# Performance work log

Measured on AMD Instinct MI355X. Metric: run time of the kernel, lower is better.

The kernel has to match this reference:

```python
import jax, jax.numpy as jnp
import numpy as np

NUM_E = 1024
E_DIM = 64
BETA = 0.5


def setup_inputs() -> dict:
    key = jax.random.key(0)
    k1, k2 = jax.random.split(key)
    z_e = jax.random.normal(k1, (32, E_DIM, 64, 64), dtype=jnp.float32)  # [B, C, H, W]
    codebook = jax.random.uniform(k2, (NUM_E, E_DIM), dtype=jnp.float32,
                                  minval=-1.0 / NUM_E, maxval=1.0 / NUM_E)
    return {"z_e": z_e, "codebook": codebook}


def reference(z_e, codebook):
    B, C, H, W = z_e.shape
    sg = jax.lax.stop_gradient
    z = jnp.transpose(z_e, (0, 2, 3, 1))            # [B, H, W, C]
    zf = z.reshape(-1, C)                           # [N, C]
    # squared L2 distances via ||z||^2 + ||e||^2 - 2 z.e  -> [N, num_e]
    d = (jnp.sum(zf * zf, axis=1, keepdims=True)
         + jnp.sum(codebook * codebook, axis=1)
         - 2.0 * jnp.matmul(zf, codebook.T))
    idx = jnp.argmin(d, axis=1)                     # [N]
    z_q = codebook[idx].reshape(z.shape)            # gather instead of one-hot matmul
    loss = jnp.mean((sg(z_q) - z) ** 2) + BETA * jnp.mean((z_q - sg(z)) ** 2)
    z_q_st = z + sg(z_q - z)                        # straight-through
    # code usage histogram == mean of one-hot encodings
    counts = jnp.zeros((NUM_E,), dtype=z.dtype).at[idx].add(1.0)
    e_mean = counts / idx.shape[0]
    perplexity = jnp.exp(-jnp.sum(e_mean * jnp.log(e_mean + 1e-10)))
    z_q_out = jnp.transpose(z_q_st, (0, 3, 1, 2))   # back to [B, C, H, W]
    return (z_q_out, loss, sg(perplexity), idx.reshape(B, H, W))
```

## Files before the change

### kernel.cpp

```cpp
#include <hip/hip_runtime.h>
#include <math.h>

#define NUM_E   1024
#define ZQ_ELEM 8388608
#define AGRID   1024
#define QCAP    2048

typedef short bf16x8 __attribute__((ext_vector_type(8)));
typedef float f32x16 __attribute__((ext_vector_type(16)));

__device__ inline unsigned short rne_bf16(float v) {
    unsigned u = __float_as_uint(v);
    return (unsigned short)((u + 0x7FFFu + ((u >> 16) & 1u)) >> 16);
}

__global__ __launch_bounds__(256) void vq_prep(const float* __restrict__ cb,
                                               float* __restrict__ ee,
                                               unsigned short* __restrict__ ehi)
{
    int j = blockIdx.x * 256 + threadIdx.x;
    const float* r = cb + (size_t)j * 64;
    float v[64];
#pragma unroll
    for (int k = 0; k < 64; ++k) v[k] = r[k];
    float a = 0.f;
#pragma unroll
    for (int k = 0; k < 64; ++k) a = fmaf(v[k], v[k], a);
    ee[j] = a;

    int nt = j >> 5, jc = j & 31;
#pragma unroll
    for (int kt = 0; kt < 4; ++kt)
#pragma unroll
        for (int h = 0; h < 2; ++h) {
            bf16x8 vh;
#pragma unroll
            for (int i = 0; i < 8; ++i)
                vh[i] = (short)rne_bf16(v[kt * 16 + h * 8 + i]);
            *(bf16x8*)(ehi + ((size_t)(nt * 4 + kt) * 64 + h * 32 + jc) * 8) = vh;
        }
}

__device__ inline void refine_one(const float* zb, const float* zzs,
                                  const float* ee, const float* cb,
                                  unsigned long long* best, int pl, int j)
{
    const float4* cr = (const float4*)(cb + ((size_t)j << 6));
    float a = 0.f;
#pragma unroll
    for (int q = 0; q < 16; ++q) {
        float4 c4 = cr[q];
        a = fmaf(zb[(size_t)(4 * q + 0) * 4096 + pl], c4.x, a);
        a = fmaf(zb[(size_t)(4 * q + 1) * 4096 + pl], c4.y, a);
        a = fmaf(zb[(size_t)(4 * q + 2) * 4096 + pl], c4.z, a);
        a = fmaf(zb[(size_t)(4 * q + 3) * 4096 + pl], c4.w, a);
    }
    float t1 = zzs[pl] + ee[j];
    float d  = fmaf(-2.f, a, t1);
    unsigned long long key =
        ((unsigned long long)__float_as_uint(d) << 32) | (unsigned long long)j;
    atomicMin(best + pl, key);
}

#define LOADB(H, EV, ntv) do {                                      \
    int _b = (ntv) * 4 * 64 + lane;                                 \
    _Pragma("unroll")                                               \
    for (int _k = 0; _k < 4; ++_k) H[_k] = eh8[_b + _k * 64];       \
    EV = ee[(ntv) * 32 + (lane & 31)];                              \
} while (0)

__global__ __launch_bounds__(256, 4) void vq_argmin(
    const float* __restrict__ z, const float* __restrict__ cb,
    const unsigned short* __restrict__ ehi, const float* __restrict__ ee,
    float* __restrict__ idx_f, int* __restrict__ counts,
    float* __restrict__ zq, double* __restrict__ partials)
{
    __shared__ float zzs[128];
    __shared__ float wp[128];
    __shared__ unsigned long long best[128];
    __shared__ unsigned int queue[QCAP];
    __shared__ unsigned int qcnt;
    __shared__ unsigned int oflow;
    __shared__ int ibuf[128];
    __shared__ double wsum[4];

    const int tid  = threadIdx.x;
    const int g    = blockIdx.x;
    const int lane = tid & 63, wv = tid >> 6;
    const size_t zoff = ((size_t)(g >> 5) << 18) + (size_t)((g & 31) << 7);
    const float* zb = z + zoff;
    const bf16x8* eh8 = (const bf16x8*)ehi;

    if (tid < 128) best[tid] = 0xFFFFFFFFFFFFFFFFull;
    if (tid == 0) { qcnt = 0; oflow = 0; }

    if (tid < 128) {
        float vv[64];
#pragma unroll
        for (int k = 0; k < 64; ++k) vv[k] = zb[(size_t)k * 4096 + tid];
        float a = 0.f;
#pragma unroll
        for (int k = 0; k < 64; ++k) a = fmaf(vv[k], vv[k], a);
        zzs[tid] = a;
    }

    bf16x8 ah[4];
    {
        int h = lane >> 5;
        int pl = wv * 32 + (lane & 31);
        float s1 = 0.f, sd = 0.f;
#pragma unroll
        for (int kt = 0; kt < 4; ++kt)
#pragma unroll
            for (int i = 0; i < 8; ++i) {
                int k = kt * 16 + h * 8 + i;
                float x = zb[(size_t)k * 4096 + pl];
                unsigned short hb = rne_bf16(x);
                float hf = __uint_as_float((unsigned)hb << 16);
                ah[kt][i] = (short)hb;
                s1 += fabsf(x);
                sd += fabsf(x - hf);
            }
        s1 += __shfl_xor(s1, 32);
        sd += __shfl_xor(sd, 32);
        if (lane < 32) wp[pl] = 4.f * (s1 * 1.907e-6f + sd * 9.785e-4f) + 1.4e-4f;
    }
    __syncthreads();

    float m[16];
#pragma unroll
    for (int r = 0; r < 16; ++r) m[r] = 3.4e38f;

    bf16x8 hA[4], hB[4];
    float  eA, eB;

    LOADB(hA, eA, 0);
#pragma unroll 1
    for (int nt = 0; nt < 32; nt += 2) {
        LOADB(hB, eB, nt + 1);
        {
            f32x16 acc;
#pragma unroll
            for (int r = 0; r < 16; ++r) acc[r] = 0.f;
#pragma unroll
            for (int kt = 0; kt < 4; ++kt)
                acc = __builtin_amdgcn_mfma_f32_32x32x16_bf16(ah[kt], hA[kt], acc, 0, 0, 0);
#pragma unroll
            for (int r = 0; r < 16; ++r) m[r] = fminf(m[r], fmaf(-2.f, acc[r], eA));
        }
        if (nt + 2 < 32) LOADB(hA, eA, nt + 2);
        {
            f32x16 acc;
#pragma unroll
            for (int r = 0; r < 16; ++r) acc[r] = 0.f;
#pragma unroll
            for (int kt = 0; kt < 4; ++kt)
                acc = __builtin_amdgcn_mfma_f32_32x32x16_bf16(ah[kt], hB[kt], acc, 0, 0, 0);
#pragma unroll
            for (int r = 0; r < 16; ++r) m[r] = fminf(m[r], fmaf(-2.f, acc[r], eB));
        }
    }
#pragma unroll
    for (int r = 0; r < 16; ++r) {
        for (int d2 = 1; d2 <= 16; d2 <<= 1)
            m[r] = fminf(m[r], __shfl_xor(m[r], d2));
        m[r] += wp[wv * 32 + 4 * (lane >> 5) + (r & 3) + 8 * (r >> 2)];
    }

    LOADB(hA, eA, 0);
#pragma unroll 1
    for (int nt = 0; nt < 32; nt += 2) {
        LOADB(hB, eB, nt + 1);
        {
            f32x16 acc;
#pragma unroll
            for (int r = 0; r < 16; ++r) acc[r] = 0.f;
#pragma unroll
            for (int kt = 0; kt < 4; ++kt)
                acc = __builtin_amdgcn_mfma_f32_32x32x16_bf16(ah[kt], hA[kt], acc, 0, 0, 0);
            unsigned jj = (unsigned)(nt * 32 + (lane & 31));
#pragma unroll
            for (int r = 0; r < 16; ++r) {
                bool hit = fmaf(-2.f, acc[r], eA) <= m[r];
                if (__any(hit)) {
                    if (hit) {
                        int pl = wv * 32 + 4 * (lane >> 5) + (r & 3) + 8 * (r >> 2);
                        unsigned slot = atomicAdd(&qcnt, 1u);
                        if (slot < QCAP) queue[slot] = ((unsigned)pl << 16) | jj;
                        else oflow = 1;
                    }
                }
            }
        }
        if (nt + 2 < 32) LOADB(hA, eA, nt + 2);
        {
            f32x16 acc;
#pragma unroll
            for (int r = 0; r < 16; ++r) acc[r] = 0.f;
#pragma unroll
            for (int kt = 0; kt < 4; ++kt)
                acc = __builtin_amdgcn_mfma_f32_32x32x16_bf16(ah[kt], hB[kt], acc, 0, 0, 0);
            unsigned jj = (unsigned)((nt + 1) * 32 + (lane & 31));
#pragma unroll
            for (int r = 0; r < 16; ++r) {
                bool hit = fmaf(-2.f, acc[r], eB) <= m[r];
                if (__any(hit)) {
                    if (hit) {
                        int pl = wv * 32 + 4 * (lane >> 5) + (r & 3) + 8 * (r >> 2);
                        unsigned slot = atomicAdd(&qcnt, 1u);
                        if (slot < QCAP) queue[slot] = ((unsigned)pl << 16) | jj;
                        else oflow = 1;
                    }
                }
            }
        }
    }
    __syncthreads();

    if (oflow) {
        if (tid < 128)
            for (int j = 0; j < NUM_E; ++j) refine_one(zb, zzs, ee, cb, best, tid, j);
    } else {
        int nq = (int)qcnt;
        for (int e = tid; e < nq; e += 256) {
            unsigned u = queue[e];
            refine_one(zb, zzs, ee, cb, best, (int)(u >> 16), (int)(u & 0xFFFFu));
        }
    }
    __syncthreads();
    if (tid < 128) {
        int bi = (int)(best[tid] & 0xFFFFFFFFull);
        ibuf[tid] = bi;
        idx_f[(size_t)g * 128 + tid] = (float)bi;
        atomicAdd(&counts[bi], 1);
    }
    __syncthreads();

    {
        int w4 = tid & 31, c8 = (tid >> 5) * 8;
        const float4* zb4 = (const float4*)zb;
        float4* zq4 = (float4*)(zq + zoff);
        size_t b0 = (size_t)ibuf[w4 * 4 + 0] << 6;
        size_t b1 = (size_t)ibuf[w4 * 4 + 1] << 6;
        size_t b2 = (size_t)ibuf[w4 * 4 + 2] << 6;
        size_t b3 = (size_t)ibuf[w4 * 4 + 3] << 6;
        double ls = 0.0;
#pragma unroll
        for (int i = 0; i < 8; ++i) {
            int c = c8 + i;
            float4 zv = zb4[(size_t)c * 1024 + w4];
            float q0 = cb[b0 + c], q1 = cb[b1 + c], q2 = cb[b2 + c], q3 = cb[b3 + c];
            float t0 = q0 - zv.x, t1 = q1 - zv.y, t2 = q2 - zv.z, t3 = q3 - zv.w;
            zq4[(size_t)c * 1024 + w4] =
                make_float4(zv.x + t0, zv.y + t1, zv.z + t2, zv.w + t3);
            ls += (double)t0 * t0 + (double)t1 * t1 + (double)t2 * t2 + (double)t3 * t3;
        }
#pragma unroll
        for (int off = 32; off > 0; off >>= 1) ls += __shfl_down(ls, off);
        if ((tid & 63) == 0) wsum[tid >> 6] = ls;
    }
    __syncthreads();
    if (tid == 0) partials[g] = wsum[0] + wsum[1] + wsum[2] + wsum[3];
}

__global__ __launch_bounds__(256) void vq_final(
    const int* __restrict__ counts, const double* __restrict__ partials,
    float* __restrict__ scalars)
{
    __shared__ double sh[256];
    __shared__ double sl[256];
    int t = threadIdx.x;
    double s = 0.0;
    for (int j = t; j < NUM_E; j += 256) {
        float em   = (float)counts[j] * (1.0f / 131072.0f);
        float term = em * logf(em + 1e-10f);
        s += (double)term;
    }
    double l = 0.0;
#pragma unroll
    for (int j = 0; j < AGRID / 256; ++j) l += partials[j * 256 + t];
    sh[t] = s;
    sl[t] = l;
    __syncthreads();
    for (int off = 128; off > 0; off >>= 1) {
        if (t < off) { sh[t] += sh[t + off]; sl[t] += sl[t + off]; }
        __syncthreads();
    }
    if (t == 0) {
        float mm = (float)(sl[0] / 8388608.0);
        scalars[0] = mm + 0.5f * mm;
        scalars[1] = expf(-(float)sh[0]);
    }
}

extern "C" void kernel_launch(void* const* d_in, const int* in_sizes, int n_in,
                              void* d_out, int out_size, void* d_ws, size_t ws_size,
                              hipStream_t stream)
{
    const float* z  = (const float*)d_in[0];
    const float* cb = (const float*)d_in[1];
    float* out     = (float*)d_out;
    float* zq      = out;
    float* scalars = out + ZQ_ELEM;
    float* idx_f   = out + ZQ_ELEM + 2;

    int*            counts   = (int*)d_ws;
    double*         partials = (double*)((char*)d_ws + 4096);
    float*          ee       = (float*)((char*)d_ws + 12288);
    unsigned short* ehi      = (unsigned short*)((char*)d_ws + 16384);

    hipMemsetAsync(d_ws, 0, 4096, stream);
    vq_prep  <<<4,     256, 0, stream>>>(cb, ee, ehi);
    vq_argmin<<<AGRID, 256, 0, stream>>>(z, cb, ehi, ee, idx_f, counts, zq, partials);
    vq_final <<<1,     256, 0, stream>>>(counts, partials, scalars);
}
```

Baseline: 111.9 us.

## Stage bf16 codebook in LDS, widen blocks to 512 points with per-point candidate lists

```diff
diff --git a/kernel.cpp b/kernel.cpp
--- a/kernel.cpp
+++ b/kernel.cpp
@@ -3,8 +3,9 @@
 
 #define NUM_E   1024
 #define ZQ_ELEM 8388608
-#define AGRID   1024
-#define QCAP    2048
+#define AGRID   256
+#define MAXC    7
+#define OQCAP   512
 
 typedef short bf16x8 __attribute__((ext_vector_type(8)));
 typedef float f32x16 __attribute__((ext_vector_type(16)));
@@ -41,9 +42,26 @@
         }
 }
 
-__device__ inline void refine_one(const float* zb, const float* zzs,
-                                  const float* ee, const float* cb,
-                                  unsigned long long* best, int pl, int j)
+__device__ inline unsigned long long key_regs(const float* vv, float zz, float eej,
+                                              const float* cb, int j)
+{
+    const float4* cr = (const float4*)(cb + ((size_t)j << 6));
+    float a = 0.f;
+#pragma unroll
+    for (int q = 0; q < 16; ++q) {
+        float4 c4 = cr[q];
+        a = fmaf(vv[4 * q + 0], c4.x, a);
+        a = fmaf(vv[4 * q + 1], c4.y, a);
+        a = fmaf(vv[4 * q + 2], c4.z, a);
+        a = fmaf(vv[4 * q + 3], c4.w, a);
+    }
+    float t1 = zz + eej;
+    float d  = fmaf(-2.f, a, t1);
+    return ((unsigned long long)__float_as_uint(d) << 32) | (unsigned long long)j;
+}
+
+__device__ inline unsigned long long key_glob(const float* zb, float zz, float eej,
+                                              const float* cb, int pl, int j)
 {
     const float4* cr = (const float4*)(cb + ((size_t)j << 6));
     float a = 0.f;
@@ -55,212 +73,220 @@
         a = fmaf(zb[(size_t)(4 * q + 2) * 4096 + pl], c4.z, a);
         a = fmaf(zb[(size_t)(4 * q + 3) * 4096 + pl], c4.w, a);
     }
-    float t1 = zzs[pl] + ee[j];
+    float t1 = zz + eej;
     float d  = fmaf(-2.f, a, t1);
-    unsigned long long key =
-        ((unsigned long long)__float_as_uint(d) << 32) | (unsigned long long)j;
-    atomicMin(best + pl, key);
-}
-
-#define LOADB(H, EV, ntv) do {                                      \
-    int _b = (ntv) * 4 * 64 + lane;                                 \
-    _Pragma("unroll")                                               \
-    for (int _k = 0; _k < 4; ++_k) H[_k] = eh8[_b + _k * 64];       \
-    EV = ee[(ntv) * 32 + (lane & 31)];                              \
-} while (0)
-
-__global__ __launch_bounds__(256, 4) void vq_argmin(
+    return ((unsigned long long)__float_as_uint(d) << 32) | (unsigned long long)j;
+}
+
+__global__ __launch_bounds__(512, 2) void vq_argmin(
     const float* __restrict__ z, const float* __restrict__ cb,
     const unsigned short* __restrict__ ehi, const float* __restrict__ ee,
     float* __restrict__ idx_f, int* __restrict__ counts,
     float* __restrict__ zq, double* __restrict__ partials)
 {
-    __shared__ float zzs[128];
-    __shared__ float wp[128];
-    __shared__ unsigned long long best[128];
-    __shared__ unsigned int queue[QCAP];
-    __shared__ unsigned int qcnt;
-    __shared__ unsigned int oflow;
-    __shared__ int ibuf[128];
-    __shared__ double wsum[4];
+    __shared__ bf16x8 bB[8192];
+    __shared__ float  eeL[1024];
+    __shared__ float  zzsL[512];
+    __shared__ float  wp[512];
+    __shared__ unsigned long long best[512];
+    __shared__ unsigned short cand[512 * MAXC];
+    __shared__ unsigned int ccnt[512];
+    __shared__ unsigned int oq[OQCAP];
+    __shared__ unsigned int oqcnt, gflow;
+    __shared__ double wsum[8];
 
     const int tid  = threadIdx.x;
     const int g    = blockIdx.x;
     const int lane = tid & 63, wv = tid >> 6;
-    const size_t zoff = ((size_t)(g >> 5) << 18) + (size_t)((g & 31) << 7);
+    const size_t zoff = ((size_t)(g >> 3) << 18) + (size_t)((g & 7) << 9);
     const float* zb = z + zoff;
-    const bf16x8* eh8 = (const bf16x8*)ehi;
-
-    if (tid < 128) best[tid] = 0xFFFFFFFFFFFFFFFFull;
-    if (tid == 0) { qcnt = 0; oflow = 0; }
-
-    if (tid < 128) {
-        float vv[64];
-#pragma unroll
-        for (int k = 0; k < 64; ++k) vv[k] = zb[(size_t)k * 4096 + tid];
+
+    best[tid] = 0xFFFFFFFFFFFFFFFFull;
+    ccnt[tid] = 0;
+    if (tid == 0) { oqcnt = 0; gflow = 0; }
+    eeL[tid]       = ee[tid];
+    eeL[tid + 512] = ee[tid + 512];
+
+    {
+        const uint4* src = (const uint4*)ehi;
+        uint4* dst = (uint4*)bB;
+#pragma unroll
+        for (int pass = 0; pass < 4; ++pass) {
+            uint4 a = src[pass * 2048 + tid];
+            uint4 b = src[pass * 2048 + 512 + tid];
+            uint4 c = src[pass * 2048 + 1024 + tid];
+            uint4 d = src[pass * 2048 + 1536 + tid];
+            dst[pass * 2048 + tid] = a;
+            dst[pass * 2048 + 512 + tid] = b;
+            dst[pass * 2048 + 1024 + tid] = c;
+            dst[pass * 2048 + 1536 + tid] = d;
+        }
+    }
+
+    float vv[64];
+#pragma unroll
+    for (int k = 0; k < 64; ++k) vv[k] = zb[(size_t)k * 4096 + tid];
+    float zz;
+    {
         float a = 0.f;
 #pragma unroll
         for (int k = 0; k < 64; ++k) a = fmaf(vv[k], vv[k], a);
-        zzs[tid] = a;
-    }
-
-    bf16x8 ah[4];
+        zz = a; zzsL[tid] = a;
+    }
+
+    bf16x8 ah0[4], ah1[4];
     {
         int h = lane >> 5;
-        int pl = wv * 32 + (lane & 31);
-        float s1 = 0.f, sd = 0.f;
-#pragma unroll
-        for (int kt = 0; kt < 4; ++kt)
-#pragma unroll
-            for (int i = 0; i < 8; ++i) {
-                int k = kt * 16 + h * 8 + i;
-                float x = zb[(size_t)k * 4096 + pl];
-                unsigned short hb = rne_bf16(x);
-                float hf = __uint_as_float((unsigned)hb << 16);
-                ah[kt][i] = (short)hb;
-                s1 += fabsf(x);
-                sd += fabsf(x - hf);
-            }
-        s1 += __shfl_xor(s1, 32);
-        sd += __shfl_xor(sd, 32);
-        if (lane < 32) wp[pl] = 4.f * (s1 * 1.907e-6f + sd * 9.785e-4f) + 1.4e-4f;
-    }
-    __syncthreads();
-
-    float m[16];
-#pragma unroll
-    for (int r = 0; r < 16; ++r) m[r] = 3.4e38f;
-
-    bf16x8 hA[4], hB[4];
-    float  eA, eB;
-
-    LOADB(hA, eA, 0);
+#pragma unroll
+        for (int g2 = 0; g2 < 2; ++g2) {
+            int pl = wv * 64 + g2 * 32 + (lane & 31);
+            float s1 = 0.f, sd = 0.f;
+#pragma unroll
+            for (int kt = 0; kt < 4; ++kt)
+#pragma unroll
+                for (int i = 0; i < 8; ++i) {
+                    int k = kt * 16 + h * 8 + i;
+                    float x = zb[(size_t)k * 4096 + pl];
+                    unsigned short hb = rne_bf16(x);
+                    float hf = __uint_as_float((unsigned)hb << 16);
+                    if (g2 == 0) ah0[kt][i] = (short)hb; else ah1[kt][i] = (short)hb;
+                    s1 += fabsf(x);
+                    sd += fabsf(x - hf);
+                }
+            s1 += __shfl_xor(s1, 32);
+            sd += __shfl_xor(sd, 32);
+            if (lane < 32) wp[pl] = 4.f * (s1 * 1.907e-6f + sd * 9.785e-4f) + 1.4e-4f;
+        }
+    }
+    __syncthreads();
+
+    float m0[16], m1[16];
+#pragma unroll
+    for (int r = 0; r < 16; ++r) { m0[r] = 3.4e38f; m1[r] = 3.4e38f; }
+
+#pragma unroll 2
+    for (int nt = 0; nt < 32; ++nt) {
+        bf16x8 b0 = bB[(nt * 4 + 0) * 64 + lane];
+        bf16x8 b1 = bB[(nt * 4 + 1) * 64 + lane];
+        bf16x8 b2 = bB[(nt * 4 + 2) * 64 + lane];
+        bf16x8 b3 = bB[(nt * 4 + 3) * 64 + lane];
+        float eA = eeL[nt * 32 + (lane & 31)];
+        f32x16 a0, a1;
+#pragma unroll
+        for (int r = 0; r < 16; ++r) { a0[r] = 0.f; a1[r] = 0.f; }
+        a0 = __builtin_amdgcn_mfma_f32_32x32x16_bf16(ah0[0], b0, a0, 0, 0, 0);
+        a1 = __builtin_amdgcn_mfma_f32_32x32x16_bf16(ah1[0], b0, a1, 0, 0, 0);
+        a0 = __builtin_amdgcn_mfma_f32_32x32x16_bf16(ah0[1], b1, a0, 0, 0, 0);
+        a1 = __builtin_amdgcn_mfma_f32_32x32x16_bf16(ah1[1], b1, a1, 0, 0, 0);
+        a0 = __builtin_amdgcn_mfma_f32_32x32x16_bf16(ah0[2], b2, a0, 0, 0, 0);
+        a1 = __builtin_amdgcn_mfma_f32_32x32x16_bf16(ah1[2], b2, a1, 0, 0, 0);
+        a0 = __builtin_amdgcn_mfma_f32_32x32x16_bf16(ah0[3], b3, a0, 0, 0, 0);
+        a1 = __builtin_amdgcn_mfma_f32_32x32x16_bf16(ah1[3], b3, a1, 0, 0, 0);
+#pragma unroll
+        for (int r = 0; r < 16; ++r) {
+            m0[r] = fminf(m0[r], fmaf(-2.f, a0[r], eA));
+            m1[r] = fminf(m1[r], fmaf(-2.f, a1[r], eA));
+        }
+    }
+#pragma unroll
+    for (int r = 0; r < 16; ++r) {
+        for (int d2 = 1; d2 <= 16; d2 <<= 1) {
+            m0[r] = fminf(m0[r], __shfl_xor(m0[r], d2));
+            m1[r] = fminf(m1[r], __shfl_xor(m1[r], d2));
+        }
+        int row = 4 * (lane >> 5) + (r & 3) + 8 * (r >> 2);
+        m0[r] += wp[wv * 64 + row];
+        m1[r] += wp[wv * 64 + 32 + row];
+    }
+
+#define ENQ(PL, JJ) do {                                                  \
+    unsigned _s = atomicAdd(&ccnt[PL], 1u);                               \
+    if (_s < MAXC) cand[(PL) * MAXC + _s] = (unsigned short)(JJ);         \
+    else { unsigned _o = atomicAdd(&oqcnt, 1u);                           \
+           if (_o < OQCAP) oq[_o] = ((unsigned)(PL) << 16) | (JJ);        \
+           else gflow = 1; }                                              \
+} while (0)
+
 #pragma unroll 1
-    for (int nt = 0; nt < 32; nt += 2) {
-        LOADB(hB, eB, nt + 1);
-        {
-            f32x16 acc;
-#pragma unroll
-            for (int r = 0; r < 16; ++r) acc[r] = 0.f;
-#pragma unroll
-            for (int kt = 0; kt < 4; ++kt)
-                acc = __builtin_amdgcn_mfma_f32_32x32x16_bf16(ah[kt], hA[kt], acc, 0, 0, 0);
-#pragma unroll
-            for (int r = 0; r < 16; ++r) m[r] = fminf(m[r], fmaf(-2.f, acc[r], eA));
-        }
-        if (nt + 2 < 32) LOADB(hA, eA, nt + 2);
-        {
-            f32x16 acc;
-#pragma unroll
-            for (int r = 0; r < 16; ++r) acc[r] = 0.f;
-#pragma unroll
-            for (int kt = 0; kt < 4; ++kt)
-                acc = __builtin_amdgcn_mfma_f32_32x32x16_bf16(ah[kt], hB[kt], acc, 0, 0, 0);
-#pragma unroll
-            for (int r = 0; r < 16; ++r) m[r] = fminf(m[r], fmaf(-2.f, acc[r], eB));
-        }
-    }
-#pragma unroll
-    for (int r = 0; r < 16; ++r) {
-        for (int d2 = 1; d2 <= 16; d2 <<= 1)
-            m[r] = fminf(m[r], __shfl_xor(m[r], d2));
-        m[r] += wp[wv * 32 + 4 * (lane >> 5) + (r & 3) + 8 * (r >> 2)];
-    }
-
-    LOADB(hA, eA, 0);
-#pragma unroll 1
-    for (int nt = 0; nt < 32; nt += 2) {
-        LOADB(hB, eB, nt + 1);
-        {
-            f32x16 acc;
-#pragma unroll
-            for (int r = 0; r < 16; ++r) acc[r] = 0.f;
-#pragma unroll
-            for (int kt = 0; kt < 4; ++kt)
-                acc = __builtin_amdgcn_mfma_f32_32x32x16_bf16(ah[kt], hA[kt], acc, 0, 0, 0);
-            unsigned jj = (unsigned)(nt * 32 + (lane & 31));
-#pragma unroll
-            for (int r = 0; r < 16; ++r) {
-                bool hit = fmaf(-2.f, acc[r], eA) <= m[r];
-                if (__any(hit)) {
-                    if (hit) {
-                        int pl = wv * 32 + 4 * (lane >> 5) + (r & 3) + 8 * (r >> 2);
-                        unsigned slot = atomicAdd(&qcnt, 1u);
-                        if (slot < QCAP) queue[slot] = ((unsigned)pl << 16) | jj;
-                        else oflow = 1;
-                    }
-                }
-            }
-        }
-        if (nt + 2 < 32) LOADB(hA, eA, nt + 2);
-        {
-            f32x16 acc;
-#pragma unroll
-            for (int r = 0; r < 16; ++r) acc[r] = 0.f;
-#pragma unroll
-            for (int kt = 0; kt < 4; ++kt)
-                acc = __builtin_amdgcn_mfma_f32_32x32x16_bf16(ah[kt], hB[kt], acc, 0, 0, 0);
-            unsigned jj = (unsigned)((nt + 1) * 32 + (lane & 31));
-#pragma unroll
-            for (int r = 0; r < 16; ++r) {
-                bool hit = fmaf(-2.f, acc[r], eB) <= m[r];
-                if (__any(hit)) {
-                    if (hit) {
-                        int pl = wv * 32 + 4 * (lane >> 5) + (r & 3) + 8 * (r >> 2);
-                        unsigned slot = atomicAdd(&qcnt, 1u);
-                        if (slot < QCAP) queue[slot] = ((unsigned)pl << 16) | jj;
-                        else oflow = 1;
-                    }
-                }
-            }
-        }
-    }
-    __syncthreads();
-
-    if (oflow) {
-        if (tid < 128)
-            for (int j = 0; j < NUM_E; ++j) refine_one(zb, zzs, ee, cb, best, tid, j);
+    for (int nt = 0; nt < 32; ++nt) {
+        bf16x8 b0 = bB[(nt * 4 + 0) * 64 + lane];
+        bf16x8 b1 = bB[(nt * 4 + 1) * 64 + lane];
+        bf16x8 b2 = bB[(nt * 4 + 2) * 64 + lane];
+        bf16x8 b3 = bB[(nt * 4 + 3) * 64 + lane];
+        float eA = eeL[nt * 32 + (lane & 31)];
+        f32x16 a0, a1;
+#pragma unroll
+        for (int r = 0; r < 16; ++r) { a0[r] = 0.f; a1[r] = 0.f; }
+        a0 = __builtin_amdgcn_mfma_f32_32x32x16_bf16(ah0[0], b0, a0, 0, 0, 0);
+        a1 = __builtin_amdgcn_mfma_f32_32x32x16_bf16(ah1[0], b0, a1, 0, 0, 0);
+        a0 = __builtin_amdgcn_mfma_f32_32x32x16_bf16(ah0[1], b1, a0, 0, 0, 0);
+        a1 = __builtin_amdgcn_mfma_f32_32x32x16_bf16(ah1[1], b1, a1, 0, 0, 0);
+        a0 = __builtin_amdgcn_mfma_f32_32x32x16_bf16(ah0[2], b2, a0, 0, 0, 0);
+        a1 = __builtin_amdgcn_mfma_f32_32x32x16_bf16(ah1[2], b2, a1, 0, 0, 0);
+        a0 = __builtin_amdgcn_mfma_f32_32x32x16_bf16(ah0[3], b3, a0, 0, 0, 0);
+        a1 = __builtin_amdgcn_mfma_f32_32x32x16_bf16(ah1[3], b3, a1, 0, 0, 0);
+        unsigned jj = (unsigned)(nt * 32 + (lane & 31));
+#pragma unroll
+        for (int r = 0; r < 16; ++r) {
+            int row = 4 * (lane >> 5) + (r & 3) + 8 * (r >> 2);
+            bool h0 = fmaf(-2.f, a0[r], eA) <= m0[r];
+            if (__any(h0)) { if (h0) { int pl = wv * 64 + row;      ENQ(pl, jj); } }
+            bool h1 = fmaf(-2.f, a1[r], eA) <= m1[r];
+            if (__any(h1)) { if (h1) { int pl = wv * 64 + 32 + row; ENQ(pl, jj); } }
+        }
+    }
+    __syncthreads();
+
+    if (gflow) {
+        unsigned long long bk = 0xFFFFFFFFFFFFFFFFull;
+        for (int j = 0; j < NUM_E; ++j) {
+            unsigned long long k2 = key_regs(vv, zz, eeL[j], cb, j);
+            if (k2 < bk) bk = k2;
+        }
+        best[tid] = bk;
     } else {
-        int nq = (int)qcnt;
-        for (int e = tid; e < nq; e += 256) {
-            unsigned u = queue[e];
-            refine_one(zb, zzs, ee, cb, best, (int)(u >> 16), (int)(u & 0xFFFFu));
-        }
-    }
-    __syncthreads();
-    if (tid < 128) {
+        int n = (int)ccnt[tid]; if (n > MAXC) n = MAXC;
+        unsigned long long bk = 0xFFFFFFFFFFFFFFFFull;
+        for (int e = 0; e < n; ++e) {
+            int j = (int)cand[tid * MAXC + e];
+            unsigned long long k2 = key_regs(vv, zz, eeL[j], cb, j);
+            if (k2 < bk) bk = k2;
+        }
+        atomicMin(&best[tid], bk);
+        int no = (int)oqcnt; if (no > OQCAP) no = OQCAP;
+        for (int e = tid; e < no; e += 512) {
+            unsigned u = oq[e];
+            int pl = (int)(u >> 16), j = (int)(u & 0xFFFFu);
+            atomicMin(&best[pl], key_glob(zb, zzsL[pl], eeL[j], cb, pl, j));
+        }
+    }
+    __syncthreads();
+
+    {
         int bi = (int)(best[tid] & 0xFFFFFFFFull);
-        ibuf[tid] = bi;
-        idx_f[(size_t)g * 128 + tid] = (float)bi;
+        idx_f[(size_t)g * 512 + tid] = (float)bi;
         atomicAdd(&counts[bi], 1);
-    }
-    __syncthreads();
-
-    {
-        int w4 = tid & 31, c8 = (tid >> 5) * 8;
-        const float4* zb4 = (const float4*)zb;
-        float4* zq4 = (float4*)(zq + zoff);
-        size_t b0 = (size_t)ibuf[w4 * 4 + 0] << 6;
-        size_t b1 = (size_t)ibuf[w4 * 4 + 1] << 6;
-        size_t b2 = (size_t)ibuf[w4 * 4 + 2] << 6;
-        size_t b3 = (size_t)ibuf[w4 * 4 + 3] << 6;
+        const float* crow = cb + ((size_t)bi << 6);
+        float* zqp = zq + zoff + tid;
         double ls = 0.0;
 #pragma unroll
-        for (int i = 0; i < 8; ++i) {
-            int c = c8 + i;
-            float4 zv = zb4[(size_t)c * 1024 + w4];
-            float q0 = cb[b0 + c], q1 = cb[b1 + c], q2 = cb[b2 + c], q3 = cb[b3 + c];
-            float t0 = q0 - zv.x, t1 = q1 - zv.y, t2 = q2 - zv.z, t3 = q3 - zv.w;
-            zq4[(size_t)c * 1024 + w4] =
-                make_float4(zv.x + t0, zv.y + t1, zv.z + t2, zv.w + t3);
-            ls += (double)t0 * t0 + (double)t1 * t1 + (double)t2 * t2 + (double)t3 * t3;
+        for (int c = 0; c < 64; ++c) {
+            float q = crow[c];
+            float t = q - vv[c];
+            zqp[(size_t)c * 4096] = vv[c] + t;
+            ls += (double)t * t;
         }
 #pragma unroll
         for (int off = 32; off > 0; off >>= 1) ls += __shfl_down(ls, off);
-        if ((tid & 63) == 0) wsum[tid >> 6] = ls;
-    }
-    __syncthreads();
-    if (tid == 0) partials[g] = wsum[0] + wsum[1] + wsum[2] + wsum[3];
+        if (lane == 0) wsum[wv] = ls;
+    }
+    __syncthreads();
+    if (tid == 0) {
+        double s = 0.0;
+#pragma unroll
+        for (int i = 0; i < 8; ++i) s += wsum[i];
+        partials[g] = s;
+    }
 }
 
 __global__ __launch_bounds__(256) void vq_final(
@@ -311,6 +337,6 @@
 
     hipMemsetAsync(d_ws, 0, 4096, stream);
     vq_prep  <<<4,     256, 0, stream>>>(cb, ee, ehi);
-    vq_argmin<<<AGRID, 256, 0, stream>>>(z, cb, ehi, ee, idx_f, counts, zq, partials);
+    vq_argmin<<<AGRID, 512, 0, stream>>>(z, cb, ehi, ee, idx_f, counts, zq, partials);
     vq_final <<<1,     256, 0, stream>>>(counts, partials, scalars);
 }
```

Measured after the change: 122.8 us. 9.8% more time.
